# Kernel tuning notes

Measured on AMD Instinct MI355X. Metric: run time of the kernel, lower is better.

The kernel has to match this reference:

```python
import jax, jax.numpy as jnp
import numpy as np

B, N, H, O = 262144, 64, 256, 64
MAX_ITER = 30
TOL = 1e-7
NU = 1.0


def setup_inputs() -> dict:
    key = jax.random.key(0)
    kx, kr, k1, k2, k3, k4 = jax.random.split(key, 6)
    x = jax.random.normal(kx, (B, N), dtype=jnp.float32) * 3.0
    r = jax.random.uniform(kr, (N,), dtype=jnp.float32) + 0.5  # positive rates in [0.5, 1.5)
    # MLP params (torch Linear: y = x @ W.T + b), Kaiming-ish scaling
    W1 = jax.random.normal(k1, (H, N), dtype=jnp.float32) * (1.0 / np.sqrt(N))
    b1 = jax.random.normal(k2, (H,), dtype=jnp.float32) * 0.01
    W2 = jax.random.normal(k3, (O, H), dtype=jnp.float32) * (1.0 / np.sqrt(H))
    b2 = jax.random.normal(k4, (O,), dtype=jnp.float32) * 0.01
    return {"x": x, "r": r, "W1": W1, "b1": b1, "W2": W2, "b2": b2}


def _solve_s(x, r):
    """Vectorized Newton solve of sum_i e^{-2 r_i s} x_i^2 = 1 per sample.

    Replicates solve_s_single: s starts at 0, up to MAX_ITER Newton steps,
    frozen once |F(s)| < TOL; all-zero samples return s = 0.
    """
    x2 = x * x  # [B, N]
    zero_mask = jnp.all(jnp.abs(x) <= 1e-12, axis=1)  # torch.allclose(x, 0, atol=1e-12)

    def body(_, s):
        e = jnp.exp(-2.0 * r[None, :] * s[:, None])        # [B, N]
        val = jnp.sum(e * x2, axis=1) - 1.0                # F(s)     [B]
        dval = jnp.sum(-2.0 * r[None, :] * e * x2, axis=1) # F'(s)    [B]
        safe_d = jnp.where(dval == 0.0, 1.0, dval)
        step = val / safe_d
        step = jnp.where((jnp.abs(val) < TOL) | zero_mask, 0.0, step)
        return s - step

    s0 = jnp.zeros(x.shape[0], dtype=x.dtype)
    return jax.lax.fori_loop(0, MAX_ITER, body, s0)


def reference(x, r, W1, b1, W2, b2):
    S = _solve_s(x, r)[:, None]                 # [B, 1], detached in torch (built via .item())
    S = jax.lax.stop_gradient(S)
    x_sphere = x * jnp.exp(-r[None, :] * S)     # d(-s) x
    h = jnp.maximum(x_sphere @ W1.T + b1, 0.0)  # [B, H]
    mlp_out = h @ W2.T + b2                     # [B, O]
    return mlp_out * jnp.exp(NU * S)
```

## Files before the change

### kernel.cpp

```cpp
#include <hip/hip_runtime.h>

typedef __attribute__((ext_vector_type(8))) short short8;
typedef __attribute__((ext_vector_type(4))) float floatx4;

static __device__ __forceinline__ unsigned short f2bf(float f) {
    unsigned u = __float_as_uint(f);
    u += 0x7FFFu + ((u >> 16) & 1u);
    return (unsigned short)(u >> 16);
}

__global__ __launch_bounds__(512, 2) void fused_k(const float* __restrict__ x,
                                                  const float* __restrict__ r,
                                                  const float* __restrict__ W1f,
                                                  const float* __restrict__ b1,
                                                  const float* __restrict__ W2f,
                                                  const float* __restrict__ b2,
                                                  float* __restrict__ out,
                                                  int tiles_per_block) {
    __shared__ unsigned short sW1[256 * 64];
    __shared__ unsigned short sW2[64 * 256];
    __shared__ float sB1[256];

    int tid = threadIdx.x;

    const float4* w1f4 = (const float4*)W1f;
#pragma unroll
    for (int c = 0; c < 4; ++c) {
        int g = tid + c * 512;
        int h = g >> 3, ch = g & 7;
        int prow = ((h >> 5) * 2 + ((h >> 2) & 1)) * 16 + ((h >> 3) & 3) * 4 + (h & 3);
        float4 lo = w1f4[2 * g], hi = w1f4[2 * g + 1];
        uint4 p;
        p.x = (unsigned)f2bf(lo.x) | ((unsigned)f2bf(lo.y) << 16);
        p.y = (unsigned)f2bf(lo.z) | ((unsigned)f2bf(lo.w) << 16);
        p.z = (unsigned)f2bf(hi.x) | ((unsigned)f2bf(hi.y) << 16);
        p.w = (unsigned)f2bf(hi.z) | ((unsigned)f2bf(hi.w) << 16);
        *(uint4*)&sW1[prow * 64 + (ch ^ (prow & 7)) * 8] = p;
    }
    const float4* w2f4 = (const float4*)W2f;
#pragma unroll
    for (int c = 0; c < 4; ++c) {
        int g = tid + c * 512;
        float4 lo = w2f4[2 * g], hi = w2f4[2 * g + 1];
        uint4 p;
        p.x = (unsigned)f2bf(lo.x) | ((unsigned)f2bf(lo.y) << 16);
        p.y = (unsigned)f2bf(lo.z) | ((unsigned)f2bf(lo.w) << 16);
        p.z = (unsigned)f2bf(hi.x) | ((unsigned)f2bf(hi.y) << 16);
        p.w = (unsigned)f2bf(hi.z) | ((unsigned)f2bf(hi.w) << 16);
        int row = g >> 5, ch = g & 31;
        *(uint4*)&sW2[row * 256 + (ch ^ (row & 7)) * 8] = p;
    }
    if (tid < 256) {
        int h = tid;
        int prow = ((h >> 5) * 2 + ((h >> 2) & 1)) * 16 + ((h >> 3) & 3) * 4 + (h & 3);
        sB1[prow] = b1[h];
    }
    __syncthreads();

    int wave = tid >> 6, lane = tid & 63;
    int q = lane >> 4, l16 = lane & 15;
    int sx = l16 & 7;

    float bias2[4];
#pragma unroll
    for (int n = 0; n < 4; ++n) bias2[n] = b2[n * 16 + l16];

    const float L2E2 = 2.8853900817779268f;
    float rl2[16];
    {
        const float4* r4 = (const float4*)r;
        float4 ra = r4[2 * q], rb = r4[2 * q + 1];
        float4 rc = r4[8 + 2 * q], rd = r4[8 + 2 * q + 1];
        rl2[0] = ra.x * L2E2; rl2[1] = ra.y * L2E2; rl2[2] = ra.z * L2E2; rl2[3] = ra.w * L2E2;
        rl2[4] = rb.x * L2E2; rl2[5] = rb.y * L2E2; rl2[6] = rb.z * L2E2; rl2[7] = rb.w * L2E2;
        rl2[8] = rc.x * L2E2; rl2[9] = rc.y * L2E2; rl2[10] = rc.z * L2E2; rl2[11] = rc.w * L2E2;
        rl2[12] = rd.x * L2E2; rl2[13] = rd.y * L2E2; rl2[14] = rd.z * L2E2; rl2[15] = rd.w * L2E2;
    }

    int myrow = wave * 16 + l16;
    size_t mb = (size_t)blockIdx.x * tiles_per_block * 128;
    const float4* xt = (const float4*)(x + (mb + myrow) * 64);

    float4 va = xt[2 * q], vb = xt[2 * q + 1];
    float4 vc = xt[8 + 2 * q], vd = xt[8 + 2 * q + 1];

    for (int tt = 0; tt < tiles_per_block; ++tt) {
        size_t m0 = mb + (size_t)tt * 128;

        float xv[16];
        xv[0] = va.x; xv[1] = va.y; xv[2] = va.z; xv[3] = va.w;
        xv[4] = vb.x; xv[5] = vb.y; xv[6] = vb.z; xv[7] = vb.w;
        xv[8] = vc.x; xv[9] = vc.y; xv[10] = vc.z; xv[11] = vc.w;
        xv[12] = vd.x; xv[13] = vd.y; xv[14] = vd.z; xv[15] = vd.w;

        {
            int nt = (tt + 1 < tiles_per_block) ? (tt + 1) : tt;
            const float4* xn = xt + (size_t)nt * 2048;
            va = xn[2 * q]; vb = xn[2 * q + 1];
            vc = xn[8 + 2 * q]; vd = xn[8 + 2 * q + 1];
        }

        float x2[16], rx2[16], r2x2[16];
        float sum0 = 0.f, sumr = 0.f;
        int nz = 0;
#pragma unroll
        for (int j = 0; j < 16; ++j) {
            x2[j] = xv[j] * xv[j];
            rx2[j] = rl2[j] * x2[j];
            r2x2[j] = rl2[j] * rx2[j];
            sum0 += x2[j];
            sumr += rx2[j];
            nz |= (fabsf(xv[j]) > 1e-12f) ? 1 : 0;
        }
        sum0 += __shfl_xor(sum0, 16); sum0 += __shfl_xor(sum0, 32);
        sumr += __shfl_xor(sumr, 16); sumr += __shfl_xor(sumr, 32);
        nz   |= __shfl_xor(nz, 16);   nz   |= __shfl_xor(nz, 32);

        float s = 0.f;
        if (nz) {
            s = __log2f(sum0) * sum0 * __builtin_amdgcn_rcpf(sumr);
#pragma unroll 1
            for (int it = 0; it < 8; ++it) {
                float ns = -s;
                float v = 0.f, dv = 0.f, d2 = 0.f;
#pragma unroll
                for (int j = 0; j < 16; ++j) {
                    float e = __builtin_amdgcn_exp2f(ns * rl2[j]);
                    v  = fmaf(e, x2[j], v);
                    dv = fmaf(e, rx2[j], dv);
                    d2 = fmaf(e, r2x2[j], d2);
                }
                v  += __shfl_xor(v, 16);  v  += __shfl_xor(v, 32);
                dv += __shfl_xor(dv, 16); dv += __shfl_xor(dv, 32);
                d2 += __shfl_xor(d2, 16); d2 += __shfl_xor(d2, 32);
                if (__all(fabsf(v - 1.f) < 1e-5f)) break;
                float l2v = __log2f(v);
                float rdv = __builtin_amdgcn_rcpf(dv);
                float tcor = (0.34657359f * l2v) * fmaf(d2 * v, rdv * rdv, -1.f);
                tcor = fminf(tcor, 0.7f);
                s += l2v * v * rdv * __builtin_amdgcn_rcpf(1.f - tcor);
            }
        }

        float hs = -0.5f * s;
        unsigned pa[8];
#pragma unroll
        for (int j = 0; j < 8; ++j) {
            float ea = xv[2 * j] * __builtin_amdgcn_exp2f(hs * rl2[2 * j]);
            float eb = xv[2 * j + 1] * __builtin_amdgcn_exp2f(hs * rl2[2 * j + 1]);
            asm("v_cvt_pk_bf16_f32 %0, %1, %2" : "=v"(pa[j]) : "v"(ea), "v"(eb));
        }
        int4 w0 = make_int4((int)pa[0], (int)pa[1], (int)pa[2], (int)pa[3]);
        int4 w1 = make_int4((int)pa[4], (int)pa[5], (int)pa[6], (int)pa[7]);
        short8 a0 = *(short8*)&w0;
        short8 a1 = *(short8*)&w1;

        float es = __builtin_amdgcn_exp2f(s * 1.4426950408889634f);
        float sc[4];
#pragma unroll
        for (int reg = 0; reg < 4; ++reg) sc[reg] = __shfl(es, q * 4 + reg);

        floatx4 oacc[4];
#pragma unroll
        for (int n = 0; n < 4; ++n)
            oacc[n] = (floatx4){bias2[n], bias2[n], bias2[n], bias2[n]};

#pragma unroll
        for (int hc = 0; hc < 8; ++hc) {
            unsigned pk0, pk1, pk2, pk3;
            {
                int t = hc * 2;
                int row = t * 16 + l16;
                short8 wb0 = *(const short8*)&sW1[row * 64 + (q ^ sx) * 8];
                short8 wb1 = *(const short8*)&sW1[row * 64 + ((q + 4) ^ sx) * 8];
                const float4 bb = *(const float4*)&sB1[t * 16 + q * 4];
                floatx4 acc = (floatx4){bb.x, bb.y, bb.z, bb.w};
                acc = __builtin_amdgcn_mfma_f32_16x16x32_bf16(wb0, a0, acc, 0, 0, 0);
                acc = __builtin_amdgcn_mfma_f32_16x16x32_bf16(wb1, a1, acc, 0, 0, 0);
                float h0 = fmaxf(acc[0], 0.f), h1 = fmaxf(acc[1], 0.f);
                float h2 = fmaxf(acc[2], 0.f), h3 = fmaxf(acc[3], 0.f);
                asm("v_cvt_pk_bf16_f32 %0, %1, %2" : "=v"(pk0) : "v"(h0), "v"(h1));
                asm("v_cvt_pk_bf16_f32 %0, %1, %2" : "=v"(pk1) : "v"(h2), "v"(h3));
            }
            {
                int t = hc * 2 + 1;
                int row = t * 16 + l16;
                short8 wb0 = *(const short8*)&sW1[row * 64 + (q ^ sx) * 8];
                short8 wb1 = *(const short8*)&sW1[row * 64 + ((q + 4) ^ sx) * 8];
                const float4 bb = *(const float4*)&sB1[t * 16 + q * 4];
                floatx4 acc = (floatx4){bb.x, bb.y, bb.z, bb.w};
                acc = __builtin_amdgcn_mfma_f32_16x16x32_bf16(wb0, a0, acc, 0, 0, 0);
                acc = __builtin_amdgcn_mfma_f32_16x16x32_bf16(wb1, a1, acc, 0, 0, 0);
                float h0 = fmaxf(acc[0], 0.f), h1 = fmaxf(acc[1], 0.f);
                float h2 = fmaxf(acc[2], 0.f), h3 = fmaxf(acc[3], 0.f);
                asm("v_cvt_pk_bf16_f32 %0, %1, %2" : "=v"(pk2) : "v"(h0), "v"(h1));
                asm("v_cvt_pk_bf16_f32 %0, %1, %2" : "=v"(pk3) : "v"(h2), "v"(h3));
            }
            int4 hw = make_int4((int)pk0, (int)pk1, (int)pk2, (int)pk3);
            short8 ha = *(short8*)&hw;
#pragma unroll
            for (int n = 0; n < 4; ++n) {
                int orow = n * 16 + l16;
                short8 wb = *(const short8*)&sW2[orow * 256 + ((hc * 4 + q) ^ sx) * 8];
                oacc[n] = __builtin_amdgcn_mfma_f32_16x16x32_bf16(ha, wb, oacc[n], 0, 0, 0);
            }
        }
#pragma unroll
        for (int n = 0; n < 4; ++n) {
#pragma unroll
            for (int reg = 0; reg < 4; ++reg) {
                out[(m0 + wave * 16 + q * 4 + reg) * 64 + n * 16 + l16] =
                    oacc[n][reg] * sc[reg];
            }
        }
    }
}

extern "C" void kernel_launch(void* const* d_in, const int* in_sizes, int n_in,
                              void* d_out, int out_size, void* d_ws, size_t ws_size,
                              hipStream_t stream) {
    const float* x  = (const float*)d_in[0];
    const float* r  = (const float*)d_in[1];
    const float* W1 = (const float*)d_in[2];
    const float* b1 = (const float*)d_in[3];
    const float* W2 = (const float*)d_in[4];
    const float* b2 = (const float*)d_in[5];
    float* out = (float*)d_out;
    int B = in_sizes[0] / 64;

    int tiles = B / 128;
    int blocks = 512;
    int tpb = tiles / blocks;

    fused_k<<<blocks, 512, 0, stream>>>(x, r, W1, b1, W2, b2, out, tpb);
}
```

Baseline: 140.5 us.

## Use permlane swaps for reductions and simplify Newton step in log space

Cross-lane reductions switch from __shfl_xor (ds_bpermute through LDS hardware) to permlane16/32_swap intrinsics, which exchange values directly between VGPR lanes. The Halley-style solver that also tracked the second derivative d2 becomes a plain log-space Newton step with only value and first derivative, and the iteration cap rises from 8 to 10. This drops one reduction and one array per iteration and lowers register pressure, but convergence may need more iterations.

```diff
diff --git a/kernel.cpp b/kernel.cpp
--- a/kernel.cpp
+++ b/kernel.cpp
@@ -2,11 +2,31 @@
 
 typedef __attribute__((ext_vector_type(8))) short short8;
 typedef __attribute__((ext_vector_type(4))) float floatx4;
+typedef __attribute__((ext_vector_type(2))) unsigned uint2e;
 
 static __device__ __forceinline__ unsigned short f2bf(float f) {
     unsigned u = __float_as_uint(f);
     u += 0x7FFFu + ((u >> 16) & 1u);
     return (unsigned short)(u >> 16);
+}
+
+static __device__ __forceinline__ float pl16_sum(float x) {
+    unsigned u = __float_as_uint(x);
+    uint2e p = __builtin_amdgcn_permlane16_swap(u, u, false, false);
+    return __uint_as_float(p.x) + __uint_as_float(p.y);
+}
+static __device__ __forceinline__ float pl32_sum(float x) {
+    unsigned u = __float_as_uint(x);
+    uint2e p = __builtin_amdgcn_permlane32_swap(u, u, false, false);
+    return __uint_as_float(p.x) + __uint_as_float(p.y);
+}
+static __device__ __forceinline__ int pl16_or(int x) {
+    uint2e p = __builtin_amdgcn_permlane16_swap((unsigned)x, (unsigned)x, false, false);
+    return (int)(p.x | p.y);
+}
+static __device__ __forceinline__ int pl32_or(int x) {
+    uint2e p = __builtin_amdgcn_permlane32_swap((unsigned)x, (unsigned)x, false, false);
+    return (int)(p.x | p.y);
 }
 
 __global__ __launch_bounds__(512, 2) void fused_k(const float* __restrict__ x,
@@ -100,45 +120,38 @@
             vc = xn[8 + 2 * q]; vd = xn[8 + 2 * q + 1];
         }
 
-        float x2[16], rx2[16], r2x2[16];
+        float x2[16], rx2[16];
         float sum0 = 0.f, sumr = 0.f;
         int nz = 0;
 #pragma unroll
         for (int j = 0; j < 16; ++j) {
             x2[j] = xv[j] * xv[j];
             rx2[j] = rl2[j] * x2[j];
-            r2x2[j] = rl2[j] * rx2[j];
             sum0 += x2[j];
             sumr += rx2[j];
             nz |= (fabsf(xv[j]) > 1e-12f) ? 1 : 0;
         }
-        sum0 += __shfl_xor(sum0, 16); sum0 += __shfl_xor(sum0, 32);
-        sumr += __shfl_xor(sumr, 16); sumr += __shfl_xor(sumr, 32);
-        nz   |= __shfl_xor(nz, 16);   nz   |= __shfl_xor(nz, 32);
+        sum0 = pl32_sum(pl16_sum(sum0));
+        sumr = pl32_sum(pl16_sum(sumr));
+        nz = pl32_or(pl16_or(nz));
 
         float s = 0.f;
         if (nz) {
             s = __log2f(sum0) * sum0 * __builtin_amdgcn_rcpf(sumr);
 #pragma unroll 1
-            for (int it = 0; it < 8; ++it) {
+            for (int it = 0; it < 10; ++it) {
                 float ns = -s;
-                float v = 0.f, dv = 0.f, d2 = 0.f;
+                float v = 0.f, dv = 0.f;
 #pragma unroll
                 for (int j = 0; j < 16; ++j) {
                     float e = __builtin_amdgcn_exp2f(ns * rl2[j]);
-                    v  = fmaf(e, x2[j], v);
+                    v = fmaf(e, x2[j], v);
                     dv = fmaf(e, rx2[j], dv);
-                    d2 = fmaf(e, r2x2[j], d2);
                 }
-                v  += __shfl_xor(v, 16);  v  += __shfl_xor(v, 32);
-                dv += __shfl_xor(dv, 16); dv += __shfl_xor(dv, 32);
-                d2 += __shfl_xor(d2, 16); d2 += __shfl_xor(d2, 32);
+                v = pl32_sum(pl16_sum(v));
+                dv = pl32_sum(pl16_sum(dv));
                 if (__all(fabsf(v - 1.f) < 1e-5f)) break;
-                float l2v = __log2f(v);
-                float rdv = __builtin_amdgcn_rcpf(dv);
-                float tcor = (0.34657359f * l2v) * fmaf(d2 * v, rdv * rdv, -1.f);
-                tcor = fminf(tcor, 0.7f);
-                s += l2v * v * rdv * __builtin_amdgcn_rcpf(1.f - tcor);
+                s += __log2f(v) * v * __builtin_amdgcn_rcpf(dv);
             }
         }
 
```

Result: faster. 137.3 us (-2.3%).
